# Kernel tuning notes

Measured on AMD Instinct MI355X. Metric: run time of the kernel, lower is better.

## Reference

```python
import jax, jax.numpy as jnp
import numpy as np

B, S, H, NH = 2, 2048, 1024, 16
HD = H // NH


def setup_inputs() -> dict:
    key = jax.random.key(0)
    ks = jax.random.split(key, 12)
    query = jax.random.normal(ks[0], (B, S, H), dtype=jnp.float32)
    key_t = jax.random.normal(ks[1], (B, S, H), dtype=jnp.float32)
    value = jax.random.normal(ks[2], (B, S, H), dtype=jnp.float32)
    kpm = jax.random.randint(ks[3], (B, S), 0, 2).astype(bool)
    kpm = kpm.at[:, 0].set(False)  # guarantee at least one unmasked key per row
    bias = jax.random.normal(ks[4], (1, NH, S, S), dtype=jnp.float32)
    init = 0.02
    q_w = jax.random.normal(ks[5], (H, H), dtype=jnp.float32) * init
    k_w = jax.random.normal(ks[6], (H, H), dtype=jnp.float32) * init
    v_w = jax.random.normal(ks[7], (H, H), dtype=jnp.float32) * init
    o_w = jax.random.normal(ks[8], (H, H), dtype=jnp.float32) * init
    q_b = jnp.zeros((H,), jnp.float32)
    k_b = jnp.zeros((H,), jnp.float32)
    v_b = jnp.zeros((H,), jnp.float32)
    o_b = jnp.zeros((H,), jnp.float32)
    return {"query": query, "key": key_t, "value": value,
            "key_padding_mask": kpm, "bias": bias,
            "q_w": q_w, "q_b": q_b, "k_w": k_w, "k_b": k_b,
            "v_w": v_w, "v_b": v_b, "o_w": o_w, "o_b": o_b}


def _shape(x):
    # [B, S, H] -> [B, NH, S, HD]
    b, s, _ = x.shape
    return x.reshape(b, s, NH, HD).transpose(0, 2, 1, 3)


def reference(query, key, value, key_padding_mask, bias,
              q_w, q_b, k_w, k_b, v_w, v_b, o_w, o_b):
    scale = HD ** -0.5
    q = _shape(query @ q_w.T + q_b)
    k = _shape(key @ k_w.T + k_b)
    v = _shape(value @ v_w.T + v_b)
    attn = jnp.einsum('bhqd,bhkd->bhqk', q, k) * scale + bias
    mask = key_padding_mask[:, None, None, :]  # [B,1,1,S]
    attn = jnp.where(mask, -jnp.inf, attn)
    probs = jax.nn.softmax(attn, axis=-1)
    # safe-softmax: zero masked entries and renormalize with clamped denom
    probs = jnp.where(mask, 0.0, probs)
    denom = jnp.maximum(probs.sum(axis=-1, keepdims=True), 1e-6)
    probs = probs / denom
    ctx = jnp.einsum('bhqk,bhkd->bhqd', probs, v)
    ctx = ctx.transpose(0, 2, 1, 3).reshape(query.shape[0], query.shape[1], H)
    return ctx @ o_w.T + o_b
```

## Files before the change

kernel.cpp:

```cpp
#include <hip/hip_runtime.h>
#include <math.h>

#define Ss  2048
#define Hh  1024

typedef unsigned short u16;
typedef __attribute__((ext_vector_type(8))) short short8;
typedef __attribute__((ext_vector_type(4))) float fx4;

__device__ __forceinline__ u16 f2bf(float f) {
  unsigned int u = __float_as_uint(f);
  u = (u + 0x7fffu + ((u >> 16) & 1u)) >> 16;
  return (u16)u;
}

__device__ __forceinline__ void gld_lds16(const u16* g, u16* l) {
  __builtin_amdgcn_global_load_lds(
      (const __attribute__((address_space(1))) unsigned int*)(const unsigned int*)g,
      (__attribute__((address_space(3))) unsigned int*)(unsigned int*)l, 16, 0, 0);
}

#define MFMA16(a,b,c) __builtin_amdgcn_mfma_f32_16x16x32_bf16((a),(b),(c),0,0,0)

__global__ __launch_bounds__(256) void prep(
    const float* __restrict__ q, const float* __restrict__ k,
    const float* __restrict__ v, const float* __restrict__ wq,
    const float* __restrict__ wk, const float* __restrict__ wv,
    const float* __restrict__ wo,
    u16* __restrict__ oq, u16* __restrict__ ok, u16* __restrict__ ov,
    u16* __restrict__ owq, u16* __restrict__ owk, u16* __restrict__ owv,
    u16* __restrict__ owo) {
  const int bid = blockIdx.x;
  const float* in; u16* out; int x;
  if (bid < 12288) {
    const int z = bid >> 12; x = bid & 4095;
    in = z == 0 ? q : (z == 1 ? k : v);
    out = z == 0 ? oq : (z == 1 ? ok : ov);
  } else {
    const int t = bid - 12288, z = t >> 10; x = t & 1023;
    in = z == 0 ? wq : (z == 1 ? wk : (z == 2 ? wv : wo));
    out = z == 0 ? owq : (z == 1 ? owk : (z == 2 ? owv : owo));
  }
  const int i = (x * 256 + threadIdx.x) * 4;
  const float4 vv = *(const float4*)(in + i);
  ushort4 r; r.x = f2bf(vv.x); r.y = f2bf(vv.y); r.z = f2bf(vv.z); r.w = f2bf(vv.w);
  *(ushort4*)(out + i) = r;
}

template <int MODE>
__device__ __forceinline__ void gemm_core(const u16* __restrict__ A,
    const u16* __restrict__ W, const float* __restrict__ bias,
    void* __restrict__ out, float scale) {
  __shared__ __align__(16) u16 As[2][4096];
  __shared__ __align__(16) u16 Bs[2][4096];
  const int tid = threadIdx.x;
  const int w = tid >> 6, lane = tid & 63, ln = lane & 15, quad = lane >> 4;
  const int i0 = blockIdx.y * 128, j0 = blockIdx.x * 128;
  const int wr = (w & 1) * 64, wc = (w >> 1) * 64;
  fx4 acc[4][4] = {};
  const int L0 = w * 64 + lane, L1 = L0 + 256;
  const u16* sa0 = A + (size_t)(i0 + (L0 & 127)) * 1024 + (L0 >> 7) * 8;
  const u16* sa1 = A + (size_t)(i0 + (L1 & 127)) * 1024 + (L1 >> 7) * 8;
  const u16* sb0 = W + (size_t)(j0 + (L0 & 127)) * 1024 + (L0 >> 7) * 8;
  const u16* sb1 = W + (size_t)(j0 + (L1 & 127)) * 1024 + (L1 >> 7) * 8;
  const int d0 = (w * 64) * 8, d1 = (256 + w * 64) * 8;

  gld_lds16(sa0, &As[0][d0]); gld_lds16(sa1, &As[0][d1]);
  gld_lds16(sb0, &Bs[0][d0]); gld_lds16(sb1, &Bs[0][d1]);
  __syncthreads();

  for (int k0 = 0; k0 < 1024; k0 += 32) {
    const int cur = (k0 >> 5) & 1;
    if (k0 + 32 < 1024) {
      const int nb = cur ^ 1;
      gld_lds16(sa0 + k0 + 32, &As[nb][d0]); gld_lds16(sa1 + k0 + 32, &As[nb][d1]);
      gld_lds16(sb0 + k0 + 32, &Bs[nb][d0]); gld_lds16(sb1 + k0 + 32, &Bs[nb][d1]);
    }
    short8 a[4], b[4];
#pragma unroll
    for (int t = 0; t < 4; ++t) {
      a[t] = *(const short8*)&As[cur][(quad * 128 + wr + t * 16 + ln) * 8];
      b[t] = *(const short8*)&Bs[cur][(quad * 128 + wc + t * 16 + ln) * 8];
    }
#pragma unroll
    for (int mt = 0; mt < 4; ++mt)
#pragma unroll
      for (int nt = 0; nt < 4; ++nt)
        acc[mt][nt] = MFMA16(a[mt], b[nt], acc[mt][nt]);
    __syncthreads();
  }
#pragma unroll
  for (int nt = 0; nt < 4; ++nt) {
    const int col = j0 + wc + nt * 16 + ln;
    const float bv = bias[col];
#pragma unroll
    for (int mt = 0; mt < 4; ++mt)
#pragma unroll
      for (int r = 0; r < 4; ++r) {
        const int row = i0 + wr + mt * 16 + quad * 4 + r;
        const float val = (acc[mt][nt][r] + bv) * scale;
        if (MODE == 1) {
          const int bb = row >> 11, s = row & 2047, h = col >> 6, d = col & 63;
          ((u16*)out)[((size_t)(bb * 16 + h) * 2048 + s) * 64 + d] = f2bf(val);
        } else {
          ((float*)out)[(size_t)row * 1024 + col] = val;
        }
      }
  }
}

__global__ __launch_bounds__(256) void gemm_qkv(
    const u16* xq, const u16* xk, const u16* xv,
    const u16* wq, const u16* wk, const u16* wv,
    const float* bq, const float* bk, const float* bv,
    u16* q, u16* k, u16* v) {
  const int z = blockIdx.z;
  const u16* A = z == 0 ? xq : (z == 1 ? xk : xv);
  const u16* W = z == 0 ? wq : (z == 1 ? wk : wv);
  const float* bb = z == 0 ? bq : (z == 1 ? bk : bv);
  u16* o = z == 0 ? q : (z == 1 ? k : v);
  const float sc = z == 0 ? 0.125f : 1.0f;
  gemm_core<1>(A, W, bb, o, sc);
}

__global__ __launch_bounds__(256) void gemm_o(const u16* ctx, const u16* wo,
                                              const float* ob, float* out) {
  gemm_core<0>(ctx, wo, ob, out, 1.0f);
}

__global__ __launch_bounds__(256) void transpose_v(const u16* __restrict__ v,
                                                   u16* __restrict__ vt) {
  __shared__ u16 T[64][72];
  const int tid = threadIdx.x;
  const int bh = blockIdx.y, s0 = blockIdx.x * 64;
#pragma unroll
  for (int i = 0; i < 2; ++i) {
    const int L = i * 256 + tid, key = L >> 3, dc = L & 7;
    const uint4 val = *(const uint4*)&v[((size_t)bh * 2048 + s0 + key) * 64 + dc * 8];
    *(uint4*)&T[key][dc * 8] = val;
  }
  __syncthreads();
#pragma unroll
  for (int i = 0; i < 2; ++i) {
    const int L = i * 256 + tid, d = L >> 3, kc = L & 7;
    u16 tmp[8];
#pragma unroll
    for (int j = 0; j < 8; ++j) tmp[j] = T[kc * 8 + j][d];
    *(uint4*)&vt[((size_t)bh * 64 + d) * 2048 + s0 + kc * 8] = *(const uint4*)tmp;
  }
}

__global__ __launch_bounds__(256, 4) void attn(const u16* __restrict__ Qb,
    const u16* __restrict__ Kb, const u16* __restrict__ VT,
    const float* __restrict__ bias, const int* __restrict__ kpm,
    u16* __restrict__ ctx) {
  __shared__ __align__(16) u16 Vs[2][4096];
  __shared__ __align__(16) u16 Ps[4096];
  const int tid = threadIdx.x;
  const int w = tid >> 6, lane = tid & 63, ln = lane & 15, quad = lane >> 4;
  const int q0 = blockIdx.x * 64;
  const int hb = blockIdx.y, h = hb >> 1, b = hb & 1, bh = b * 16 + h;
  const int wr = w * 16;

  short8 qf[2];
#pragma unroll
  for (int ks = 0; ks < 2; ++ks)
    qf[ks] = *(const short8*)&Qb[((size_t)bh * 2048 + q0 + wr + ln) * 64 +
                                 ks * 32 + quad * 8];
  float mi = -3.0e38f, li = 0.f;
  fx4 O[4] = {};

  const int L0 = w * 64 + lane, L1 = L0 + 256;
  const u16* sv0 = VT + ((size_t)bh * 64 + (L0 & 63)) * 2048 + (L0 >> 6) * 8;
  const u16* sv1 = VT + ((size_t)bh * 64 + (L1 & 63)) * 2048 + (L1 >> 6) * 8;
  const int d0 = (w * 64) * 8, d1 = (256 + w * 64) * 8;

  const u16* kb_l = Kb + ((size_t)bh * 2048 + ln) * 64 + quad * 8;
  const float* bp = bias + (size_t)h * Ss * Ss + (size_t)(q0 + wr + ln) * Ss + quad * 4;
  const int* mp = kpm + b * Ss + quad * 4;

  gld_lds16(sv0, &Vs[0][d0]); gld_lds16(sv1, &Vs[0][d1]);
  fx4 bm[4];
#pragma unroll
  for (int nt = 0; nt < 4; ++nt) {
    const float4 bv = *(const float4*)(bp + nt * 16);
    const int4 mv = *(const int4*)(mp + nt * 16);
    bm[nt][0] = bv.x + (mv.x ? -1.0e30f : 0.0f);
    bm[nt][1] = bv.y + (mv.y ? -1.0e30f : 0.0f);
    bm[nt][2] = bv.z + (mv.z ? -1.0e30f : 0.0f);
    bm[nt][3] = bv.w + (mv.w ? -1.0e30f : 0.0f);
  }
  __syncthreads();

  for (int kt = 0; kt < Ss; kt += 64) {
    const int cur = (kt >> 6) & 1;
    if (kt + 64 < Ss) {
      const int nb = cur ^ 1;
      gld_lds16(sv0 + kt + 64, &Vs[nb][d0]);
      gld_lds16(sv1 + kt + 64, &Vs[nb][d1]);
    }
    const int kn = (kt + 64 < Ss) ? kt + 64 : kt;
    fx4 bmn[4];
#pragma unroll
    for (int nt = 0; nt < 4; ++nt) {
      const float4 bv = *(const float4*)(bp + kn + nt * 16);
      const int4 mv = *(const int4*)(mp + kn + nt * 16);
      bmn[nt][0] = bv.x + (mv.x ? -1.0e30f : 0.0f);
      bmn[nt][1] = bv.y + (mv.y ? -1.0e30f : 0.0f);
      bmn[nt][2] = bv.z + (mv.z ? -1.0e30f : 0.0f);
      bmn[nt][3] = bv.w + (mv.w ? -1.0e30f : 0.0f);
    }

    short8 kf[2][4];
    const u16* kp8 = kb_l + (size_t)kt * 64;
#pragma unroll
    for (int ks = 0; ks < 2; ++ks)
#pragma unroll
      for (int nt = 0; nt < 4; ++nt)
        kf[ks][nt] = *(const short8*)(kp8 + nt * 1024 + ks * 32);

    fx4 S[4] = {};
#pragma unroll
    for (int ks = 0; ks < 2; ++ks)
#pragma unroll
      for (int nt = 0; nt < 4; ++nt)
        S[nt] = MFMA16(kf[ks][nt], qf[ks], S[nt]);

    float pmax = -3.0e38f;
#pragma unroll
    for (int nt = 0; nt < 4; ++nt)
#pragma unroll
      for (int r = 0; r < 4; ++r) {
        S[nt][r] += bm[nt][r];
        pmax = fmaxf(pmax, S[nt][r]);
      }
    pmax = fmaxf(pmax, __shfl_xor(pmax, 16));
    pmax = fmaxf(pmax, __shfl_xor(pmax, 32));

    if (!__all(pmax <= mi + 8.0f)) {
      const float mn = fmaxf(mi, pmax);
      const float a = __expf(mi - mn);
#pragma unroll
      for (int r = 0; r < 4; ++r) {
        const float ar = __shfl(a, quad * 4 + r);
#pragma unroll
        for (int nt = 0; nt < 4; ++nt) O[nt][r] *= ar;
      }
      li *= a;
      mi = mn;
    }

    float rs = 0.f;
#pragma unroll
    for (int nt = 0; nt < 4; ++nt)
#pragma unroll
      for (int r = 0; r < 4; ++r) {
        S[nt][r] = __expf(S[nt][r] - mi);
        rs += S[nt][r];
      }
    rs += __shfl_xor(rs, 16);
    rs += __shfl_xor(rs, 32);
    li += rs;

#pragma unroll
    for (int nt = 0; nt < 4; ++nt) {
      unsigned int u0, u1;
      asm("v_cvt_pk_bf16_f32 %0, %1, %2" : "=v"(u0) : "v"(S[nt][0]), "v"(S[nt][1]));
      asm("v_cvt_pk_bf16_f32 %0, %1, %2" : "=v"(u1) : "v"(S[nt][2]), "v"(S[nt][3]));
      const int kcb = nt * 2 + (quad >> 1);
      uint2 pk; pk.x = u0; pk.y = u1;
      *(uint2*)&Ps[(kcb * 64 + wr + ln) * 8 + (quad & 1) * 4] = pk;
    }

#pragma unroll
    for (int ks = 0; ks < 2; ++ks) {
      const short8 pf = *(const short8*)&Ps[((ks * 4 + quad) * 64 + wr + ln) * 8];
#pragma unroll
      for (int nt = 0; nt < 4; ++nt) {
        const short8 vf = *(const short8*)&Vs[cur][((ks * 4 + quad) * 64 + nt * 16 + ln) * 8];
        O[nt] = MFMA16(pf, vf, O[nt]);
      }
    }

#pragma unroll
    for (int nt = 0; nt < 4; ++nt) bm[nt] = bmn[nt];
    __syncthreads();
  }

#pragma unroll
  for (int r = 0; r < 4; ++r) {
    const float lr = __shfl(li, quad * 4 + r);
    const float inv = 1.0f / fmaxf(lr, 1e-6f);
    const int qg = q0 + wr + quad * 4 + r;
#pragma unroll
    for (int nt = 0; nt < 4; ++nt)
      ctx[((size_t)(b * Ss + qg)) * 1024 + h * 64 + nt * 16 + ln] =
          f2bf(O[nt][r] * inv);
  }
}

extern "C" void kernel_launch(void* const* d_in, const int* in_sizes, int n_in,
                              void* d_out, int out_size, void* d_ws, size_t ws_size,
                              hipStream_t stream) {
  const float* query = (const float*)d_in[0];
  const float* key   = (const float*)d_in[1];
  const float* value = (const float*)d_in[2];
  const int*   kpm   = (const int*)d_in[3];
  const float* bias  = (const float*)d_in[4];
  const float* q_w   = (const float*)d_in[5];
  const float* q_b   = (const float*)d_in[6];
  const float* k_w   = (const float*)d_in[7];
  const float* k_b   = (const float*)d_in[8];
  const float* v_w   = (const float*)d_in[9];
  const float* v_b   = (const float*)d_in[10];
  const float* o_w   = (const float*)d_in[11];
  const float* o_b   = (const float*)d_in[12];
  float* out = (float*)d_out;

  char* ws = (char*)d_ws;
  const size_t MB = 1024 * 1024;
  u16* xq = (u16*)(ws + 0 * MB);
  u16* xk = (u16*)(ws + 8 * MB);
  u16* xv = (u16*)(ws + 16 * MB);
  u16* wq = (u16*)(ws + 24 * MB);
  u16* wk = (u16*)(ws + 26 * MB);
  u16* wv = (u16*)(ws + 28 * MB);
  u16* wo = (u16*)(ws + 30 * MB);
  u16* qb = (u16*)(ws + 32 * MB);
  u16* kb = (u16*)(ws + 40 * MB);
  u16* vb = (u16*)(ws + 48 * MB);
  u16* cx = (u16*)(ws + 56 * MB);
  u16* vt = (u16*)(ws + 0 * MB);

  prep<<<dim3(16384), 256, 0, stream>>>(query, key, value, q_w, k_w, v_w, o_w,
                                        xq, xk, xv, wq, wk, wv, wo);
  gemm_qkv<<<dim3(8, 32, 3), 256, 0, stream>>>(xq, xk, xv, wq, wk, wv,
                                               q_b, k_b, v_b, qb, kb, vb);
  transpose_v<<<dim3(32, 32), 256, 0, stream>>>(vb, vt);
  attn<<<dim3(32, 32), 256, 0, stream>>>(qb, kb, vt, bias, kpm, cx);
  gemm_o<<<dim3(8, 32), 256, 0, stream>>>(cx, wo, o_b, out);
}
```

Measured before the change: 666.8 us.

## Stage K tiles in LDS for attention and shrink GEMM row tile

Result: faster. 625.9 us (-6.1%).

```diff
diff --git a/kernel.cpp b/kernel.cpp
--- a/kernel.cpp
+++ b/kernel.cpp
@@ -51,54 +51,54 @@
 __device__ __forceinline__ void gemm_core(const u16* __restrict__ A,
     const u16* __restrict__ W, const float* __restrict__ bias,
     void* __restrict__ out, float scale) {
-  __shared__ __align__(16) u16 As[2][4096];
+  __shared__ __align__(16) u16 As[2][2048];
   __shared__ __align__(16) u16 Bs[2][4096];
   const int tid = threadIdx.x;
   const int w = tid >> 6, lane = tid & 63, ln = lane & 15, quad = lane >> 4;
-  const int i0 = blockIdx.y * 128, j0 = blockIdx.x * 128;
-  const int wr = (w & 1) * 64, wc = (w >> 1) * 64;
-  fx4 acc[4][4] = {};
-  const int L0 = w * 64 + lane, L1 = L0 + 256;
-  const u16* sa0 = A + (size_t)(i0 + (L0 & 127)) * 1024 + (L0 >> 7) * 8;
-  const u16* sa1 = A + (size_t)(i0 + (L1 & 127)) * 1024 + (L1 >> 7) * 8;
-  const u16* sb0 = W + (size_t)(j0 + (L0 & 127)) * 1024 + (L0 >> 7) * 8;
-  const u16* sb1 = W + (size_t)(j0 + (L1 & 127)) * 1024 + (L1 >> 7) * 8;
-  const int d0 = (w * 64) * 8, d1 = (256 + w * 64) * 8;
-
-  gld_lds16(sa0, &As[0][d0]); gld_lds16(sa1, &As[0][d1]);
-  gld_lds16(sb0, &Bs[0][d0]); gld_lds16(sb1, &Bs[0][d1]);
+  const int i0 = blockIdx.y * 64, j0 = blockIdx.x * 128;
+  const int wc = w * 32;
+  fx4 acc[4][2] = {};
+  const u16* sa  = A + (size_t)(i0 + lane) * 1024 + w * 8;
+  const u16* sb0 = W + (size_t)(j0 + lane) * 1024 + w * 8;
+  const u16* sb1 = W + (size_t)(j0 + 64 + lane) * 1024 + w * 8;
+  const int da = w * 512, db0 = w * 1024, db1 = w * 1024 + 512;
+
+  gld_lds16(sa, &As[0][da]);
+  gld_lds16(sb0, &Bs[0][db0]); gld_lds16(sb1, &Bs[0][db1]);
   __syncthreads();
 
   for (int k0 = 0; k0 < 1024; k0 += 32) {
     const int cur = (k0 >> 5) & 1;
     if (k0 + 32 < 1024) {
       const int nb = cur ^ 1;
-      gld_lds16(sa0 + k0 + 32, &As[nb][d0]); gld_lds16(sa1 + k0 + 32, &As[nb][d1]);
-      gld_lds16(sb0 + k0 + 32, &Bs[nb][d0]); gld_lds16(sb1 + k0 + 32, &Bs[nb][d1]);
-    }
-    short8 a[4], b[4];
-#pragma unroll
-    for (int t = 0; t < 4; ++t) {
-      a[t] = *(const short8*)&As[cur][(quad * 128 + wr + t * 16 + ln) * 8];
-      b[t] = *(const short8*)&Bs[cur][(quad * 128 + wc + t * 16 + ln) * 8];
-    }
+      gld_lds16(sa + k0 + 32, &As[nb][da]);
+      gld_lds16(sb0 + k0 + 32, &Bs[nb][db0]);
+      gld_lds16(sb1 + k0 + 32, &Bs[nb][db1]);
+    }
+    short8 a[4], b[2];
+#pragma unroll
+    for (int t = 0; t < 4; ++t)
+      a[t] = *(const short8*)&As[cur][(quad * 64 + t * 16 + ln) * 8];
+#pragma unroll
+    for (int n = 0; n < 2; ++n)
+      b[n] = *(const short8*)&Bs[cur][(quad * 128 + wc + n * 16 + ln) * 8];
 #pragma unroll
     for (int mt = 0; mt < 4; ++mt)
 #pragma unroll
-      for (int nt = 0; nt < 4; ++nt)
-        acc[mt][nt] = MFMA16(a[mt], b[nt], acc[mt][nt]);
+      for (int n = 0; n < 2; ++n)
+        acc[mt][n] = MFMA16(a[mt], b[n], acc[mt][n]);
     __syncthreads();
   }
 #pragma unroll
-  for (int nt = 0; nt < 4; ++nt) {
-    const int col = j0 + wc + nt * 16 + ln;
+  for (int n = 0; n < 2; ++n) {
+    const int col = j0 + wc + n * 16 + ln;
     const float bv = bias[col];
 #pragma unroll
     for (int mt = 0; mt < 4; ++mt)
 #pragma unroll
       for (int r = 0; r < 4; ++r) {
-        const int row = i0 + wr + mt * 16 + quad * 4 + r;
-        const float val = (acc[mt][nt][r] + bv) * scale;
+        const int row = i0 + mt * 16 + quad * 4 + r;
+        const float val = (acc[mt][n][r] + bv) * scale;
         if (MODE == 1) {
           const int bb = row >> 11, s = row & 2047, h = col >> 6, d = col & 63;
           ((u16*)out)[((size_t)(bb * 16 + h) * 2048 + s) * 64 + d] = f2bf(val);
@@ -109,7 +109,7 @@
   }
 }
 
-__global__ __launch_bounds__(256) void gemm_qkv(
+__global__ __launch_bounds__(256, 4) void gemm_qkv(
     const u16* xq, const u16* xk, const u16* xv,
     const u16* wq, const u16* wk, const u16* wv,
     const float* bq, const float* bk, const float* bv,
@@ -123,8 +123,8 @@
   gemm_core<1>(A, W, bb, o, sc);
 }
 
-__global__ __launch_bounds__(256) void gemm_o(const u16* ctx, const u16* wo,
-                                              const float* ob, float* out) {
+__global__ __launch_bounds__(256, 4) void gemm_o(const u16* ctx, const u16* wo,
+                                                 const float* ob, float* out) {
   gemm_core<0>(ctx, wo, ob, out, 1.0f);
 }
 
@@ -150,10 +150,11 @@
   }
 }
 
-__global__ __launch_bounds__(256, 4) void attn(const u16* __restrict__ Qb,
+__global__ __launch_bounds__(256) void attn(const u16* __restrict__ Qb,
     const u16* __restrict__ Kb, const u16* __restrict__ VT,
     const float* __restrict__ bias, const int* __restrict__ kpm,
     u16* __restrict__ ctx) {
+  __shared__ __align__(16) u16 Ks[2][4096];
   __shared__ __align__(16) u16 Vs[2][4096];
   __shared__ __align__(16) u16 Ps[4096];
   const int tid = threadIdx.x;
@@ -171,14 +172,16 @@
   fx4 O[4] = {};
 
   const int L0 = w * 64 + lane, L1 = L0 + 256;
+  const u16* sk0 = Kb + ((size_t)bh * 2048 + (L0 & 63)) * 64 + (L0 >> 6) * 8;
+  const u16* sk1 = Kb + ((size_t)bh * 2048 + (L1 & 63)) * 64 + (L1 >> 6) * 8;
   const u16* sv0 = VT + ((size_t)bh * 64 + (L0 & 63)) * 2048 + (L0 >> 6) * 8;
   const u16* sv1 = VT + ((size_t)bh * 64 + (L1 & 63)) * 2048 + (L1 >> 6) * 8;
   const int d0 = (w * 64) * 8, d1 = (256 + w * 64) * 8;
 
-  const u16* kb_l = Kb + ((size_t)bh * 2048 + ln) * 64 + quad * 8;
   const float* bp = bias + (size_t)h * Ss * Ss + (size_t)(q0 + wr + ln) * Ss + quad * 4;
   const int* mp = kpm + b * Ss + quad * 4;
 
+  gld_lds16(sk0, &Ks[0][d0]); gld_lds16(sk1, &Ks[0][d1]);
   gld_lds16(sv0, &Vs[0][d0]); gld_lds16(sv1, &Vs[0][d1]);
   fx4 bm[4];
 #pragma unroll
@@ -196,6 +199,8 @@
     const int cur = (kt >> 6) & 1;
     if (kt + 64 < Ss) {
       const int nb = cur ^ 1;
+      gld_lds16(sk0 + (size_t)(kt + 64) * 64, &Ks[nb][d0]);
+      gld_lds16(sk1 + (size_t)(kt + 64) * 64, &Ks[nb][d1]);
       gld_lds16(sv0 + kt + 64, &Vs[nb][d0]);
       gld_lds16(sv1 + kt + 64, &Vs[nb][d1]);
     }
@@ -211,20 +216,14 @@
       bmn[nt][3] = bv.w + (mv.w ? -1.0e30f : 0.0f);
     }
 
-    short8 kf[2][4];
-    const u16* kp8 = kb_l + (size_t)kt * 64;
+    fx4 S[4] = {};
 #pragma unroll
     for (int ks = 0; ks < 2; ++ks)
 #pragma unroll
-      for (int nt = 0; nt < 4; ++nt)
-        kf[ks][nt] = *(const short8*)(kp8 + nt * 1024 + ks * 32);
-
-    fx4 S[4] = {};
-#pragma unroll
-    for (int ks = 0; ks < 2; ++ks)
-#pragma unroll
-      for (int nt = 0; nt < 4; ++nt)
-        S[nt] = MFMA16(kf[ks][nt], qf[ks], S[nt]);
+      for (int nt = 0; nt < 4; ++nt) {
+        const short8 kf = *(const short8*)&Ks[cur][((ks * 4 + quad) * 64 + nt * 16 + ln) * 8];
+        S[nt] = MFMA16(kf, qf[ks], S[nt]);
+      }
 
     float pmax = -3.0e38f;
 #pragma unroll
@@ -334,9 +333,9 @@
 
   prep<<<dim3(16384), 256, 0, stream>>>(query, key, value, q_w, k_w, v_w, o_w,
                                         xq, xk, xv, wq, wk, wv, wo);
-  gemm_qkv<<<dim3(8, 32, 3), 256, 0, stream>>>(xq, xk, xv, wq, wk, wv,
+  gemm_qkv<<<dim3(8, 64, 3), 256, 0, stream>>>(xq, xk, xv, wq, wk, wv,
                                                q_b, k_b, v_b, qb, kb, vb);
   transpose_v<<<dim3(32, 32), 256, 0, stream>>>(vb, vt);
   attn<<<dim3(32, 32), 256, 0, stream>>>(qb, kb, vt, bias, kpm, cx);
-  gemm_o<<<dim3(8, 32), 256, 0, stream>>>(cx, wo, o_b, out);
-}
+  gemm_o<<<dim3(8, 64), 256, 0, stream>>>(cx, wo, o_b, out);
+}
```

## Stage K tiles in LDS and double query tile per block to 128 rows

Applied to the files above, without the earlier changes.

Result: faster. 610.8 us (-8.4%).

```diff
diff --git a/kernel.cpp b/kernel.cpp
--- a/kernel.cpp
+++ b/kernel.cpp
@@ -150,15 +150,16 @@
   }
 }
 
-__global__ __launch_bounds__(256, 4) void attn(const u16* __restrict__ Qb,
+__global__ __launch_bounds__(512) void attn(const u16* __restrict__ Qb,
     const u16* __restrict__ Kb, const u16* __restrict__ VT,
     const float* __restrict__ bias, const int* __restrict__ kpm,
     u16* __restrict__ ctx) {
+  __shared__ __align__(16) u16 Ks[2][4096];
   __shared__ __align__(16) u16 Vs[2][4096];
-  __shared__ __align__(16) u16 Ps[4096];
+  __shared__ __align__(16) u16 Ps[8192];
   const int tid = threadIdx.x;
   const int w = tid >> 6, lane = tid & 63, ln = lane & 15, quad = lane >> 4;
-  const int q0 = blockIdx.x * 64;
+  const int q0 = blockIdx.x * 128;
   const int hb = blockIdx.y, h = hb >> 1, b = hb & 1, bh = b * 16 + h;
   const int wr = w * 16;
 
@@ -170,16 +171,22 @@
   float mi = -3.0e38f, li = 0.f;
   fx4 O[4] = {};
 
-  const int L0 = w * 64 + lane, L1 = L0 + 256;
-  const u16* sv0 = VT + ((size_t)bh * 64 + (L0 & 63)) * 2048 + (L0 >> 6) * 8;
-  const u16* sv1 = VT + ((size_t)bh * 64 + (L1 & 63)) * 2048 + (L1 >> 6) * 8;
-  const int d0 = (w * 64) * 8, d1 = (256 + w * 64) * 8;
-
-  const u16* kb_l = Kb + ((size_t)bh * 2048 + ln) * 64 + quad * 8;
+  const int wk = w & 3;
+  const u16* s0, *s1;
+  if (w < 4) {
+    s0 = Kb + ((size_t)bh * 2048 + lane) * 64 + wk * 8;
+    s1 = Kb + ((size_t)bh * 2048 + lane) * 64 + (wk + 4) * 8;
+  } else {
+    s0 = VT + ((size_t)bh * 64 + lane) * 2048 + wk * 8;
+    s1 = VT + ((size_t)bh * 64 + lane) * 2048 + (wk + 4) * 8;
+  }
+  const int dA0 = wk * 512, dA1 = 2048 + wk * 512;
+
   const float* bp = bias + (size_t)h * Ss * Ss + (size_t)(q0 + wr + ln) * Ss + quad * 4;
   const int* mp = kpm + b * Ss + quad * 4;
 
-  gld_lds16(sv0, &Vs[0][d0]); gld_lds16(sv1, &Vs[0][d1]);
+  if (w < 4) { gld_lds16(s0, &Ks[0][dA0]); gld_lds16(s1, &Ks[0][dA1]); }
+  else       { gld_lds16(s0, &Vs[0][dA0]); gld_lds16(s1, &Vs[0][dA1]); }
   fx4 bm[4];
 #pragma unroll
   for (int nt = 0; nt < 4; ++nt) {
@@ -196,8 +203,13 @@
     const int cur = (kt >> 6) & 1;
     if (kt + 64 < Ss) {
       const int nb = cur ^ 1;
-      gld_lds16(sv0 + kt + 64, &Vs[nb][d0]);
-      gld_lds16(sv1 + kt + 64, &Vs[nb][d1]);
+      if (w < 4) {
+        gld_lds16(s0 + (size_t)(kt + 64) * 64, &Ks[nb][dA0]);
+        gld_lds16(s1 + (size_t)(kt + 64) * 64, &Ks[nb][dA1]);
+      } else {
+        gld_lds16(s0 + kt + 64, &Vs[nb][dA0]);
+        gld_lds16(s1 + kt + 64, &Vs[nb][dA1]);
+      }
     }
     const int kn = (kt + 64 < Ss) ? kt + 64 : kt;
     fx4 bmn[4];
@@ -211,20 +223,14 @@
       bmn[nt][3] = bv.w + (mv.w ? -1.0e30f : 0.0f);
     }
 
-    short8 kf[2][4];
-    const u16* kp8 = kb_l + (size_t)kt * 64;
+    fx4 S[4] = {};
 #pragma unroll
     for (int ks = 0; ks < 2; ++ks)
 #pragma unroll
-      for (int nt = 0; nt < 4; ++nt)
-        kf[ks][nt] = *(const short8*)(kp8 + nt * 1024 + ks * 32);
-
-    fx4 S[4] = {};
-#pragma unroll
-    for (int ks = 0; ks < 2; ++ks)
-#pragma unroll
-      for (int nt = 0; nt < 4; ++nt)
-        S[nt] = MFMA16(kf[ks][nt], qf[ks], S[nt]);
+      for (int nt = 0; nt < 4; ++nt) {
+        const short8 kf = *(const short8*)&Ks[cur][((ks * 4 + quad) * 64 + nt * 16 + ln) * 8];
+        S[nt] = MFMA16(kf, qf[ks], S[nt]);
+      }
 
     float pmax = -3.0e38f;
 #pragma unroll
@@ -269,12 +275,12 @@
       asm("v_cvt_pk_bf16_f32 %0, %1, %2" : "=v"(u1) : "v"(S[nt][2]), "v"(S[nt][3]));
       const int kcb = nt * 2 + (quad >> 1);
       uint2 pk; pk.x = u0; pk.y = u1;
-      *(uint2*)&Ps[(kcb * 64 + wr + ln) * 8 + (quad & 1) * 4] = pk;
+      *(uint2*)&Ps[(kcb * 128 + wr + ln) * 8 + (quad & 1) * 4] = pk;
     }
 
 #pragma unroll
     for (int ks = 0; ks < 2; ++ks) {
-      const short8 pf = *(const short8*)&Ps[((ks * 4 + quad) * 64 + wr + ln) * 8];
+      const short8 pf = *(const short8*)&Ps[((ks * 4 + quad) * 128 + wr + ln) * 8];
 #pragma unroll
       for (int nt = 0; nt < 4; ++nt) {
         const short8 vf = *(const short8*)&Vs[cur][((ks * 4 + quad) * 64 + nt * 16 + ln) * 8];
@@ -337,6 +343,6 @@
   gemm_qkv<<<dim3(8, 32, 3), 256, 0, stream>>>(xq, xk, xv, wq, wk, wv,
                                                q_b, k_b, v_b, qb, kb, vb);
   transpose_v<<<dim3(32, 32), 256, 0, stream>>>(vb, vt);
-  attn<<<dim3(32, 32), 256, 0, stream>>>(qb, kb, vt, bias, kpm, cx);
+  attn<<<dim3(16, 32), 512, 0, stream>>>(qb, kb, vt, bias, kpm, cx);
   gemm_o<<<dim3(8, 32), 256, 0, stream>>>(cx, wo, o_b, out);
 }
```
